# Kernel tuning notes

Measured on AMD Instinct MI355X. Metric: run time of the kernel, lower is better.

The kernel has to match this reference:

```python
import jax, jax.numpy as jnp
import numpy as np

# ---- Mamba2 / model hyperparameters (from init_kwargs + mamba_ssm defaults) ----
D_MODEL = 64
D_STATE = 64
D_CONV = 4
EXPAND = 2
HEADDIM = 64                      # mamba_ssm Mamba2 default
D_INNER = EXPAND * D_MODEL        # 128
NHEADS = D_INNER // HEADDIM       # 2
CONV_DIM = D_INNER + 2 * D_STATE  # 256 (ngroups=1)
D_IN_PROJ = 2 * D_INNER + 2 * D_STATE + NHEADS  # 386
B, T, F_ = 4, 128, 128
EPS = 1e-5


def silu(x):
    return x * jax.nn.sigmoid(x)


def depthwise_causal_conv(x, w, b):
    # x: [N, L, C], w: [C, K], b: [C]  (causal depthwise conv, as in Mamba2)
    xt = x.transpose(0, 2, 1)           # [N, C, L]
    kernel = w[:, None, :]              # [C, 1, K]
    y = jax.lax.conv_general_dilated(
        xt, kernel, window_strides=(1,), padding=[(D_CONV - 1, 0)],
        feature_group_count=CONV_DIM)
    return y.transpose(0, 2, 1) + b     # [N, L, C]


def mamba2(u, Wp, cw, cb, dtb, Al, Dp, nw, Wo):
    # u: [N, L, D_MODEL]
    Nb, L, _ = u.shape
    zxbcdt = u @ Wp.T                                   # [N, L, D_IN_PROJ]
    z = zxbcdt[..., :D_INNER]
    xBC = zxbcdt[..., D_INNER:D_INNER + CONV_DIM]
    dt = jax.nn.softplus(zxbcdt[..., -NHEADS:] + dtb)   # [N, L, H]
    xBC = silu(depthwise_causal_conv(xBC, cw, cb))
    x = xBC[..., :D_INNER].reshape(Nb, L, NHEADS, HEADDIM)
    Bm = xBC[..., D_INNER:D_INNER + D_STATE]            # [N, L, Nst]
    Cm = xBC[..., D_INNER + D_STATE:]                   # [N, L, Nst]
    dA = jnp.exp(dt * (-jnp.exp(Al)))                   # [N, L, H]

    def step(h, inp):
        # h: [N, H, P, Nst]
        dA_t, dt_t, x_t, B_t, C_t = inp
        h = h * dA_t[:, :, None, None] + (dt_t[:, :, None] * x_t)[..., None] * B_t[:, None, None, :]
        y = jnp.einsum('bhpn,bn->bhp', h, C_t)
        return h, y

    h0 = jnp.zeros((Nb, NHEADS, HEADDIM, D_STATE), u.dtype)
    xs = (dA.transpose(1, 0, 2), dt.transpose(1, 0, 2),
          x.transpose(1, 0, 2, 3), Bm.transpose(1, 0, 2), Cm.transpose(1, 0, 2))
    _, ys = jax.lax.scan(step, h0, xs)                  # ys: [L, N, H, P]
    y = ys.transpose(1, 0, 2, 3) + Dp[None, None, :, None] * x
    y = y.reshape(Nb, L, D_INNER)
    # RMSNormGated (norm_before_gate=False): gate then rms-normalize
    g = y * silu(z)
    g = g * jax.lax.rsqrt(jnp.mean(g * g, axis=-1, keepdims=True) + EPS) * nw
    return g @ Wo.T                                     # [N, L, D_MODEL]


def bimamba(u, p_fwd, p_bwd, fW, fb):
    out_f = mamba2(u, *p_fwd)
    out_b = mamba2(u[:, ::-1], *p_bwd)[:, ::-1]
    return jnp.concatenate([out_f, out_b], axis=-1) @ fW.T + fb


def layernorm(x, w, b):
    m = jnp.mean(x, axis=-1, keepdims=True)
    v = jnp.mean((x - m) ** 2, axis=-1, keepdims=True)
    return (x - m) * jax.lax.rsqrt(v + EPS) * w + b


def setup_inputs() -> dict:
    key = jax.random.key(0)
    ks = jax.random.split(key, 12)
    inp = {
        'x': jax.random.normal(ks[0], (B, D_MODEL, T, F_), jnp.float32),
        # 4 Mamba2 instances stacked: [freq_fwd, freq_bwd, time_fwd, time_bwd]
        'in_proj_W': 0.02 * jax.random.normal(ks[1], (4, D_IN_PROJ, D_MODEL), jnp.float32),
        'conv_W': 0.1 * jax.random.normal(ks[2], (4, CONV_DIM, D_CONV), jnp.float32),
        'conv_b': jnp.zeros((4, CONV_DIM), jnp.float32),
        'dt_bias': 0.1 * jax.random.normal(ks[3], (4, NHEADS), jnp.float32),
        'A_log': jnp.log(jax.random.uniform(ks[4], (4, NHEADS), jnp.float32, 1.0, 16.0)),
        'D_param': 0.1 * jax.random.normal(ks[5], (4, NHEADS), jnp.float32),
        'norm_w': jnp.ones((4, D_INNER), jnp.float32),
        'out_W': 0.02 * jax.random.normal(ks[6], (4, D_MODEL, D_INNER), jnp.float32),
        # 2 BiMamba fusion linears: [freq, time]
        'fusion_W': 0.02 * jax.random.normal(ks[7], (2, D_MODEL, 2 * D_MODEL), jnp.float32),
        'fusion_b': jnp.zeros((2, D_MODEL), jnp.float32),
        # 2 LayerNorms: [freq, time]
        'ln_w': jnp.ones((2, D_MODEL), jnp.float32),
        'ln_b': jnp.zeros((2, D_MODEL), jnp.float32),
    }
    return inp


def reference(x, in_proj_W, conv_W, conv_b, dt_bias, A_log, D_param, norm_w, out_W,
              fusion_W, fusion_b, ln_w, ln_b):
    Bb, Cc, Tt, Ff = x.shape

    def mp(i):
        return (in_proj_W[i], conv_W[i], conv_b[i], dt_bias[i], A_log[i],
                D_param[i], norm_w[i], out_W[i])

    # ---- frequency axis scan (dilation == 1) ----
    x_freq = x.transpose(0, 2, 3, 1).reshape(Bb * Tt, Ff, Cc)
    xf_out = bimamba(layernorm(x_freq, ln_w[0], ln_b[0]), mp(0), mp(1), fusion_W[0], fusion_b[0])
    x = x + xf_out.reshape(Bb, Tt, Ff, Cc).transpose(0, 3, 1, 2)

    # ---- time axis scan ----
    x_time = x.transpose(0, 3, 2, 1).reshape(Bb * Ff, Tt, Cc)
    xt_out = bimamba(layernorm(x_time, ln_w[1], ln_b[1]), mp(2), mp(3), fusion_W[1], fusion_b[1])
    x = x + xt_out.reshape(Bb, Ff, Tt, Cc).transpose(0, 3, 2, 1)
    return x
```

## Files before the change

kernel.cpp:

```cpp
#include <hip/hip_runtime.h>

#define EPSV 1e-5f

typedef short bf16x8 __attribute__((ext_vector_type(8)));
typedef float f32x4 __attribute__((ext_vector_type(4)));

__device__ __forceinline__ float sigmoidf_(float x) {
  return 1.f / (1.f + __expf(-x));
}
__device__ __forceinline__ unsigned short f2bf(float f) {
  unsigned int u = __float_as_uint(f);
  u += 0x7fffu + ((u >> 16) & 1u);
  return (unsigned short)(u >> 16);
}
__device__ __forceinline__ float bfu(unsigned short h) {
  union { unsigned int u; float f; } t; t.u = ((unsigned int)h) << 16; return t.f;
}
__device__ __forceinline__ float bflo(unsigned int u) {
  union { unsigned int x; float f; } t; t.x = u << 16; return t.f;
}
__device__ __forceinline__ float bfhi(unsigned int u) {
  union { unsigned int x; float f; } t; t.x = u & 0xffff0000u; return t.f;
}

__global__ __launch_bounds__(256) void precomp_wc(
    const float* __restrict__ fW,
    const float* __restrict__ oW,
    float* __restrict__ Wc)
{
  const int bi = blockIdx.x;
  const int i = bi >> 3, mg = bi & 7;
  const int m = (mg << 3) + (threadIdx.x >> 5);
  const int k0 = (threadIdx.x & 31) << 2;
  const int p = i >> 1, d = i & 1;
  const float* fr = fW + p * 8192 + m * 128 + d * 64;
  const float* orow = oW + i * 8192 + k0;
  float a0 = 0.f, a1 = 0.f, a2 = 0.f, a3 = 0.f;
  for (int j = 0; j < 64; ++j) {
    const float f = fr[j];
    const float4 o4 = *(const float4*)(orow + j * 128);
    a0 += f * o4.x; a1 += f * o4.y; a2 += f * o4.z; a3 += f * o4.w;
  }
  float* out = Wc + i * 8192 + m * 128 + k0;
  out[0] = a0; out[1] = a1; out[2] = a2; out[3] = a3;
}

__global__ __launch_bounds__(256) void precomp_wcf(
    const float* __restrict__ Wc, unsigned short* __restrict__ WcF)
{
  const int ip = blockIdx.x;
  const float* src = Wc + (size_t)ip * 8192;
  unsigned short* dst = WcF + (size_t)ip * 8192;
  for (int idx = threadIdx.x; idx < 8192; idx += 256) {
    const int tile = idx >> 11;
    const int h = (idx >> 9) & 3;
    const int lane = (idx >> 3) & 63;
    const int j = idx & 7;
    const int col = lane & 15, quad = lane >> 4;
    dst[idx] = f2bf(src[(tile * 16 + col) * 128 + h * 32 + quad * 8 + j]);
  }
}

__global__ __launch_bounds__(256) void precomp_wpf(
    const float* __restrict__ Wp, unsigned short* __restrict__ WpF)
{
  const int ip = blockIdx.x;
  const float* src = Wp + (size_t)ip * 24704;
  unsigned short* dst = WpF + (size_t)ip * 25600;
  for (int idx = threadIdx.x; idx < 25600; idx += 256) {
    const int tile = idx >> 10;
    const int rem = idx & 1023;
    const int h = rem >> 9;
    const int lane = (rem >> 3) & 63;
    const int j = idx & 7;
    const int col = lane & 15, quad = lane >> 4;
    const int o = tile * 16 + col;
    const int k = h * 32 + quad * 8 + j;
    dst[idx] = (o < 386) ? f2bf(src[o * 64 + k]) : (unsigned short)0;
  }
}

__global__ __launch_bounds__(256) void transp0(
    const float* __restrict__ x, float* __restrict__ x0)
{
  __shared__ float T[64 * 132];
  const int tid = threadIdx.x, blk = blockIdx.x;
  const int b = blk >> 7, t = blk & 127;
  {
    const int c = tid >> 2, f0 = (tid & 3) << 5;
    const float* xp = x + (((size_t)(b * 64 + c) * 128 + t) << 7) + f0;
    float* tp = &T[c * 132 + f0];
    #pragma unroll
    for (int j = 0; j < 8; ++j)
      *(float4*)(tp + (j << 2)) = *(const float4*)(xp + (j << 2));
  }
  __syncthreads();
  {
    const int f = tid >> 1, cb = (tid & 1) << 5;
    float* op = x0 + (((size_t)(b * 128 + t) * 128 + f) << 6) + cb;
    #pragma unroll
    for (int j = 0; j < 32; j += 4) {
      float4 v;
      v.x = T[(cb + j + 0) * 132 + f];
      v.y = T[(cb + j + 1) * 132 + f];
      v.z = T[(cb + j + 2) * 132 + f];
      v.w = T[(cb + j + 3) * 132 + f];
      *(float4*)(op + j) = v;
    }
  }
}

__global__ __launch_bounds__(512, 4) void mamba_dir(
    const float* __restrict__ src,
    unsigned short* __restrict__ ybuf,
    const unsigned short* __restrict__ WpF,
    const unsigned short* __restrict__ WcF,
    const float* __restrict__ cwA, const float* __restrict__ cbA,
    const float* __restrict__ dtbA, const float* __restrict__ AlA,
    const float* __restrict__ DpA, const float* __restrict__ nwA,
    const float* __restrict__ lnwA, const float* __restrict__ lnbA,
    int phase)
{
  __shared__ __align__(16) unsigned short sU[16 * 72];
  __shared__ __align__(16) unsigned short sZb[16 * 136];
  __shared__ __align__(16) float sZx[16 * 260];
  __shared__ __align__(16) unsigned short sBC16[16 * 136];
  __shared__ __align__(16) unsigned short sXdT[128 * 40];
  __shared__ __align__(16) unsigned short sXwT[128 * 40];
  __shared__ __align__(16) unsigned short sBT[64 * 40];
  __shared__ __align__(16) unsigned short sSm[2 * 16 * 40];
  __shared__ __align__(16) unsigned short sH[2 * 64 * 72];
  __shared__ float sMeta[16][2][4];
  __shared__ float sDtRaw[16][2];

  const int tid = threadIdx.x;
  const int blk = blockIdx.x;
  const int seq = blk >> 1, dir = blk & 1;
  const int ip = (phase << 1) + dir;
  const float dtb0 = dtbA[ip * 2], dtb1 = dtbA[ip * 2 + 1];
  const float nA0 = -__expf(AlA[ip * 2]), nA1 = -__expf(AlA[ip * 2 + 1]);
  const float Dp0 = DpA[ip * 2], Dp1 = DpA[ip * 2 + 1];
  const int c256 = tid & 255;
  const int lh = tid >> 8;
  float ch0 = 0.f, ch1 = 0.f, ch2 = 0.f;

  const int wv = tid >> 6, lane = tid & 63;
  const int col = lane & 15, quad = lane >> 4;

  f32x4 hacc[8];
  #pragma unroll
  for (int i = 0; i < 8; ++i) hacc[i] = (f32x4){0.f, 0.f, 0.f, 0.f};

  {
    unsigned int* z;
    z = (unsigned int*)sXdT; for (int i = tid; i < 2560; i += 512) z[i] = 0u;
    z = (unsigned int*)sXwT; for (int i = tid; i < 2560; i += 512) z[i] = 0u;
    z = (unsigned int*)sBT;  for (int i = tid; i < 1280; i += 512) z[i] = 0u;
    z = (unsigned int*)sSm;  for (int i = tid; i < 640;  i += 512) z[i] = 0u;
    z = (unsigned int*)sH;   for (int i = tid; i < 4608; i += 512) z[i] = 0u;
  }

  const unsigned short* wf = WpF + (size_t)ip * 25600;
  const unsigned short* wcf = WcF + (size_t)ip * 8192;
  const size_t sb = (size_t)seq << 13;
  const int pos = tid >> 6, lc = tid & 63;

  float vc0, vc1;
  {
    const int p0 = dir ? (127 - pos) : pos;
    const int p1 = dir ? (127 - (pos + 8)) : (pos + 8);
    vc0 = src[sb + (size_t)p0 * 64 + lc];
    vc1 = src[sb + (size_t)p1 * 64 + lc];
  }

  for (int ck = 0; ck < 8; ++ck) {
    float vn0 = 0.f, vn1 = 0.f;
    if (ck < 7) {
      const int st0 = ((ck + 1) << 4) + pos;
      const int p0 = dir ? (127 - st0) : st0;
      const int p1 = dir ? (127 - (st0 + 8)) : (st0 + 8);
      vn0 = src[sb + (size_t)p0 * 64 + lc];
      vn1 = src[sb + (size_t)p1 * 64 + lc];
    }
    {
      const int lnb_i = (phase << 6) + lc;
      const float lnw_v = lnwA[lnb_i], lnb_v = lnbA[lnb_i];
      #pragma unroll
      for (int half = 0; half < 2; ++half) {
        const float v = half ? vc1 : vc0;
        float sm = v, s2 = v * v;
        sm += __shfl_xor(sm, 1);  s2 += __shfl_xor(s2, 1);
        sm += __shfl_xor(sm, 2);  s2 += __shfl_xor(s2, 2);
        sm += __shfl_xor(sm, 4);  s2 += __shfl_xor(s2, 4);
        sm += __shfl_xor(sm, 8);  s2 += __shfl_xor(s2, 8);
        sm += __shfl_xor(sm, 16); s2 += __shfl_xor(s2, 16);
        sm += __shfl_xor(sm, 32); s2 += __shfl_xor(s2, 32);
        const float mean = sm * (1.f / 64.f);
        const float inv = rsqrtf(s2 * (1.f / 64.f) - mean * mean + EPSV);
        sU[(pos + half * 8) * 72 + lc] = f2bf((v - mean) * inv * lnw_v + lnb_v);
      }
    }
    __syncthreads();
    {
      const int wave = tid >> 6;
      const bf16x8 a0 = *(const bf16x8*)(&sU[col * 72 + quad * 8]);
      const bf16x8 a1 = *(const bf16x8*)(&sU[col * 72 + quad * 8 + 32]);
      for (int tile = wave; tile < 25; tile += 8) {
        const unsigned short* wt = wf + (tile << 10) + (lane << 3);
        const bf16x8 b0 = *(const bf16x8*)(wt);
        const bf16x8 b1 = *(const bf16x8*)(wt + 512);
        f32x4 d = {0.f, 0.f, 0.f, 0.f};
        d = __builtin_amdgcn_mfma_f32_16x16x32_bf16(a0, b0, d, 0, 0, 0);
        d = __builtin_amdgcn_mfma_f32_16x16x32_bf16(a1, b1, d, 0, 0, 0);
        const int o = (tile << 4) + col;
        if (tile < 8) {
          #pragma unroll
          for (int r = 0; r < 4; ++r)
            sZb[(quad * 4 + r) * 136 + o] = f2bf(d[r]);
        } else if (tile < 24) {
          #pragma unroll
          for (int r = 0; r < 4; ++r)
            sZx[(quad * 4 + r) * 260 + (o - 128)] = d[r];
        } else if (col < 2) {
          #pragma unroll
          for (int r = 0; r < 4; ++r)
            sDtRaw[quad * 4 + r][col] = d[r];
        }
      }
    }
    __syncthreads();
    {
      const int c = c256;
      const float4 cw4 = *(const float4*)(cwA + ip * 1024 + (c << 2));
      const float cbias = cbA[ip * 256 + c];
      float a0c, a1c, a2c;
      if (lh == 0) { a0c = ch0; a1c = ch1; a2c = ch2; }
      else {
        a0c = sZx[5 * 260 + c];
        a1c = sZx[6 * 260 + c];
        a2c = sZx[7 * 260 + c];
      }
      const int lt0 = lh << 3;
      unsigned int pkv[4];
      #pragma unroll
      for (int l = 0; l < 8; ++l) {
        const int lt = lt0 + l;
        const float a3 = sZx[lt * 260 + c];
        const float acc = cbias + a0c * cw4.x + a1c * cw4.y + a2c * cw4.z + a3 * cw4.w;
        const float sv = acc * sigmoidf_(acc);
        const unsigned int hv = (unsigned int)f2bf(sv);
        if (c >= 192)      sBC16[lt * 136 + 64 + (c - 192)] = (unsigned short)hv;
        else if (c >= 128) sBC16[lt * 136 + (c - 128)] = (unsigned short)hv;
        if (l & 1) pkv[l >> 1] |= hv << 16; else pkv[l >> 1] = hv;
        a0c = a1c; a1c = a2c; a2c = a3;
      }
      if (c < 128)
        *(uint4*)(&sXdT[c * 40 + lt0]) = make_uint4(pkv[0], pkv[1], pkv[2], pkv[3]);
      else if (c < 192)
        *(uint4*)(&sBT[(c - 128) * 40 + lt0]) = make_uint4(pkv[0], pkv[1], pkv[2], pkv[3]);
      if (lh == 0) {
        ch0 = sZx[13 * 260 + c];
        ch1 = sZx[14 * 260 + c];
        ch2 = sZx[15 * 260 + c];
      }
      if (tid < 32) {
        const int lt = tid >> 1, hh = tid & 1;
        const float rawv = sDtRaw[lt][hh] + (hh ? dtb1 : dtb0);
        const float dtv = (rawv > 20.f) ? rawv : log1pf(__expf(rawv));
        float Lx = dtv * (hh ? nA1 : nA0);
        #pragma unroll
        for (int d = 2; d < 32; d <<= 1) {
          const float tpv = __shfl_up(Lx, d);
          Lx += (tid >= d) ? tpv : 0.f;
        }
        const float Ltot = __shfl(Lx, 30 + hh);
        *(float4*)(&sMeta[lt][hh][0]) =
            make_float4(Lx, dtv, __expf(Ltot - Lx) * dtv, __expf(Lx));
      }
    }
    __syncthreads();
    f32x4 yD0, yD1;
    if (wv == 0) {
      const bf16x8 ca0 = *(const bf16x8*)(&sBC16[col * 136 + 64 + quad * 8]);
      const bf16x8 ca1 = *(const bf16x8*)(&sBC16[col * 136 + 96 + quad * 8]);
      const bf16x8 bb0 = *(const bf16x8*)(&sBC16[col * 136 + quad * 8]);
      const bf16x8 bb1 = *(const bf16x8*)(&sBC16[col * 136 + 32 + quad * 8]);
      f32x4 g = {0.f, 0.f, 0.f, 0.f};
      g = __builtin_amdgcn_mfma_f32_16x16x32_bf16(ca0, bb0, g, 0, 0, 0);
      g = __builtin_amdgcn_mfma_f32_16x16x32_bf16(ca1, bb1, g, 0, 0, 0);
      #pragma unroll
      for (int h = 0; h < 2; ++h) {
        const float Ls = sMeta[col][h][0];
        const float dts = sMeta[col][h][1];
        #pragma unroll
        for (int r = 0; r < 4; ++r) {
          const int t = quad * 4 + r;
          const float m = (col <= t) ? __expf(sMeta[t][h][0] - Ls) * dts : 0.f;
          sSm[(h * 16 + t) * 40 + col] = f2bf(g[r] * m);
        }
      }
    } else if (wv <= 2) {
      if (ck < 7) {
        const int p = ((wv - 1) << 6) + lane;
        const int hh = p >> 6;
        #pragma unroll
        for (int tp = 0; tp < 8; ++tp) {
          const unsigned int xr = *(const unsigned int*)(&sXdT[p * 40 + tp * 2]);
          const unsigned int lo = (unsigned int)f2bf(bflo(xr) * sMeta[tp * 2][hh][2]);
          const unsigned int hi = (unsigned int)f2bf(bfhi(xr) * sMeta[tp * 2 + 1][hh][2]);
          *(unsigned int*)(&sXwT[p * 40 + tp * 2]) = lo | (hi << 16);
        }
      }
    } else if (wv >= 4) {
      const int h = (wv - 4) >> 1, pt2 = (wv - 4) & 1;
      const bf16x8 ca0 = *(const bf16x8*)(&sBC16[col * 136 + 64 + quad * 8]);
      const bf16x8 ca1 = *(const bf16x8*)(&sBC16[col * 136 + 96 + quad * 8]);
      const unsigned short* hp0 = &sH[(h * 64 + pt2 * 32 + col) * 72];
      const unsigned short* hp1 = hp0 + 16 * 72;
      const bf16x8 h00 = *(const bf16x8*)(hp0 + quad * 8);
      const bf16x8 h01 = *(const bf16x8*)(hp0 + 32 + quad * 8);
      const bf16x8 h10 = *(const bf16x8*)(hp1 + quad * 8);
      const bf16x8 h11 = *(const bf16x8*)(hp1 + 32 + quad * 8);
      yD0 = (f32x4){0.f, 0.f, 0.f, 0.f};
      yD1 = (f32x4){0.f, 0.f, 0.f, 0.f};
      yD0 = __builtin_amdgcn_mfma_f32_16x16x32_bf16(ca0, h00, yD0, 0, 0, 0);
      yD0 = __builtin_amdgcn_mfma_f32_16x16x32_bf16(ca1, h01, yD0, 0, 0, 0);
      yD1 = __builtin_amdgcn_mfma_f32_16x16x32_bf16(ca0, h10, yD1, 0, 0, 0);
      yD1 = __builtin_amdgcn_mfma_f32_16x16x32_bf16(ca1, h11, yD1, 0, 0, 0);
      #pragma unroll
      for (int r = 0; r < 4; ++r) {
        const float Pv = sMeta[quad * 4 + r][h][3];
        yD0[r] *= Pv; yD1[r] *= Pv;
      }
    }
    __syncthreads();
    if (wv < 4) {
      if (ck < 7) {
        const int h = wv >> 1, ph = wv & 1;
        const int pb = h * 64 + ph * 32;
        const float At = sMeta[15][h][3];
        const bf16x8 xa0 = *(const bf16x8*)(&sXwT[(pb + col) * 40 + quad * 8]);
        const bf16x8 xa1 = *(const bf16x8*)(&sXwT[(pb + 16 + col) * 40 + quad * 8]);
        #pragma unroll
        for (int nt = 0; nt < 4; ++nt) {
          const bf16x8 bbt = *(const bf16x8*)(&sBT[(nt * 16 + col) * 40 + quad * 8]);
          #pragma unroll
          for (int r = 0; r < 4; ++r) { hacc[nt][r] *= At; hacc[nt + 4][r] *= At; }
          hacc[nt]     = __builtin_amdgcn_mfma_f32_16x16x32_bf16(xa0, bbt, hacc[nt], 0, 0, 0);
          hacc[nt + 4] = __builtin_amdgcn_mfma_f32_16x16x32_bf16(xa1, bbt, hacc[nt + 4], 0, 0, 0);
        }
        #pragma unroll
        for (int nt = 0; nt < 4; ++nt) {
          #pragma unroll
          for (int r = 0; r < 4; ++r) {
            sH[(pb + quad * 4 + r) * 72 + nt * 16 + col] = f2bf(hacc[nt][r]);
            sH[(pb + 16 + quad * 4 + r) * 72 + nt * 16 + col] = f2bf(hacc[nt + 4][r]);
          }
        }
      }
    } else {
      const int h = (wv - 4) >> 1, pt2 = (wv - 4) & 1;
      const int cb0 = h * 64 + pt2 * 32;
      const float dp = h ? Dp1 : Dp0;
      const bf16x8 sa = *(const bf16x8*)(&sSm[(h * 16 + col) * 40 + quad * 8]);
      const bf16x8 xb0 = *(const bf16x8*)(&sXdT[(cb0 + col) * 40 + quad * 8]);
      const bf16x8 xb1 = *(const bf16x8*)(&sXdT[(cb0 + 16 + col) * 40 + quad * 8]);
      yD0 = __builtin_amdgcn_mfma_f32_16x16x32_bf16(sa, xb0, yD0, 0, 0, 0);
      yD1 = __builtin_amdgcn_mfma_f32_16x16x32_bf16(sa, xb1, yD1, 0, 0, 0);
      const uint2 xw0 = *(const uint2*)(&sXdT[(cb0 + col) * 40 + quad * 4]);
      const uint2 xw1 = *(const uint2*)(&sXdT[(cb0 + 16 + col) * 40 + quad * 4]);
      yD0[0] += dp * bflo(xw0.x); yD0[1] += dp * bfhi(xw0.x);
      yD0[2] += dp * bflo(xw0.y); yD0[3] += dp * bfhi(xw0.y);
      yD1[0] += dp * bflo(xw1.x); yD1[1] += dp * bfhi(xw1.x);
      yD1[2] += dp * bflo(xw1.y); yD1[3] += dp * bfhi(xw1.y);
      #pragma unroll
      for (int r = 0; r < 4; ++r) {
        sZx[(quad * 4 + r) * 260 + cb0 + col] = yD0[r];
        sZx[(quad * 4 + r) * 260 + cb0 + 16 + col] = yD1[r];
      }
    }
    __syncthreads();
    {
      const int w = tid >> 6, kk = tid & 63, k0 = kk << 1;
      const float2 nw2 = *(const float2*)(nwA + ip * 128 + k0);
      #pragma unroll
      for (int sub = 0; sub < 2; ++sub) {
        const int lt = w + (sub << 3);
        const float2 yv = *(const float2*)(&sZx[lt * 260 + k0]);
        const unsigned int zp = *(const unsigned int*)(&sZb[lt * 136 + k0]);
        const float z0 = bflo(zp), z1 = bfhi(zp);
        const float g0 = yv.x * (z0 * sigmoidf_(z0));
        const float g1 = yv.y * (z1 * sigmoidf_(z1));
        float ssq = g0 * g0 + g1 * g1;
        ssq += __shfl_xor(ssq, 1);
        ssq += __shfl_xor(ssq, 2);
        ssq += __shfl_xor(ssq, 4);
        ssq += __shfl_xor(ssq, 8);
        ssq += __shfl_xor(ssq, 16);
        ssq += __shfl_xor(ssq, 32);
        const float sc = rsqrtf(ssq * (1.f / 128.f) + EPSV);
        const unsigned int lo = f2bf(g0 * sc * nw2.x);
        const unsigned int hi = f2bf(g1 * sc * nw2.y);
        *(unsigned int*)(&sZb[lt * 136 + k0]) = lo | (hi << 16);
      }
    }
    __syncthreads();
    {
      const int wave = tid >> 6;
      if (wave < 4) {
        const unsigned short* wt = wcf + (wave << 11);
        f32x4 d = {0.f, 0.f, 0.f, 0.f};
        #pragma unroll
        for (int h = 0; h < 4; ++h) {
          const bf16x8 a = *(const bf16x8*)(&sZb[col * 136 + (h << 5) + (quad << 3)]);
          const bf16x8 bb = *(const bf16x8*)(wt + (h << 9) + (lane << 3));
          d = __builtin_amdgcn_mfma_f32_16x16x32_bf16(a, bb, d, 0, 0, 0);
        }
        const size_t yb = ((size_t)(dir * 512 + seq) * 128) << 6;
        #pragma unroll
        for (int r = 0; r < 4; ++r) {
          const int pp = (quad << 2) + r;
          const int st = (ck << 4) + pp, rp = dir ? (127 - st) : st;
          ybuf[yb + ((size_t)rp << 6) + (wave << 4) + col] = f2bf(d[r]);
        }
      }
    }
    vc0 = vn0; vc1 = vn1;
  }
}

__global__ __launch_bounds__(256) void combine0(
    const float* __restrict__ x, const unsigned short* __restrict__ ybuf,
    const float* __restrict__ fb, float* __restrict__ x1)
{
  __shared__ float T[64 * 132];
  const int tid = threadIdx.x, blk = blockIdx.x;
  const int b = blk >> 7, t = blk & 127;
  {
    const int c = tid >> 2, f0 = (tid & 3) << 5;
    const float* xp = x + (((size_t)(b * 64 + c) * 128 + t) << 7) + f0;
    float* tp = &T[c * 132 + f0];
    #pragma unroll
    for (int j = 0; j < 8; ++j)
      *(float4*)(tp + (j << 2)) = *(const float4*)(xp + (j << 2));
  }
  __syncthreads();
  {
    const int f = tid >> 1, cb = (tid & 1) << 5;
    const size_t s0 = (size_t)b * 128 + t;
    const unsigned short* yf = ybuf + ((s0 * 128 + f) << 6) + cb;
    const unsigned short* yb = ybuf + (((s0 + 512) * 128 + f) << 6) + cb;
    float* op = x1 + (((size_t)(b * 128 + f) * 128 + t) << 6) + cb;
    #pragma unroll
    for (int j = 0; j < 32; j += 4) {
      float4 v;
      v.x = T[(cb + j + 0) * 132 + f] + bfu(yf[j + 0]) + bfu(yb[j + 0]) + fb[cb + j + 0];
      v.y = T[(cb + j + 1) * 132 + f] + bfu(yf[j + 1]) + bfu(yb[j + 1]) + fb[cb + j + 1];
      v.z = T[(cb + j + 2) * 132 + f] + bfu(yf[j + 2]) + bfu(yb[j + 2]) + fb[cb + j + 2];
      v.w = T[(cb + j + 3) * 132 + f] + bfu(yf[j + 3]) + bfu(yb[j + 3]) + fb[cb + j + 3];
      *(float4*)(op + j) = v;
    }
  }
}

__global__ __launch_bounds__(256) void combine1(
    const float* __restrict__ x1, const unsigned short* __restrict__ ybuf,
    const float* __restrict__ fb, float* __restrict__ out)
{
  __shared__ float T[128 * 68];
  const int tid = threadIdx.x, blk = blockIdx.x;
  const int b = blk >> 7, t = blk & 127;
  {
    const int f = tid >> 1, cb = (tid & 1) << 5;
    const size_t s1 = (size_t)b * 128 + f;
    const float* xp = x1 + ((s1 * 128 + t) << 6) + cb;
    const unsigned short* yf = ybuf + ((s1 * 128 + t) << 6) + cb;
    const unsigned short* yb = ybuf + (((s1 + 512) * 128 + t) << 6) + cb;
    float* tp = &T[f * 68 + cb];
    #pragma unroll
    for (int j = 0; j < 32; j += 4) {
      const float4 xv = *(const float4*)(xp + j);
      const uint2 yfv = *(const uint2*)(yf + j);
      const uint2 ybv = *(const uint2*)(yb + j);
      const float4 fv = *(const float4*)(fb + cb + j);
      tp[j + 0] = xv.x + bflo(yfv.x) + bflo(ybv.x) + fv.x;
      tp[j + 1] = xv.y + bfhi(yfv.x) + bfhi(ybv.x) + fv.y;
      tp[j + 2] = xv.z + bflo(yfv.y) + bflo(ybv.y) + fv.z;
      tp[j + 3] = xv.w + bfhi(yfv.y) + bfhi(ybv.y) + fv.w;
    }
  }
  __syncthreads();
  {
    const int c = tid >> 2, f0 = (tid & 3) << 5;
    float* op = out + (((size_t)(b * 64 + c) * 128 + t) << 7) + f0;
    #pragma unroll
    for (int j = 0; j < 32; j += 4) {
      float4 v;
      v.x = T[(f0 + j + 0) * 68 + c];
      v.y = T[(f0 + j + 1) * 68 + c];
      v.z = T[(f0 + j + 2) * 68 + c];
      v.w = T[(f0 + j + 3) * 68 + c];
      *(float4*)(op + j) = v;
    }
  }
}

extern "C" void kernel_launch(void* const* d_in, const int* in_sizes, int n_in,
                              void* d_out, int out_size, void* d_ws, size_t ws_size,
                              hipStream_t stream) {
  const float* x   = (const float*)d_in[0];
  const float* Wp  = (const float*)d_in[1];
  const float* cw  = (const float*)d_in[2];
  const float* cb  = (const float*)d_in[3];
  const float* dtb = (const float*)d_in[4];
  const float* Al  = (const float*)d_in[5];
  const float* Dp  = (const float*)d_in[6];
  const float* nw  = (const float*)d_in[7];
  const float* oW  = (const float*)d_in[8];
  const float* fW  = (const float*)d_in[9];
  const float* fb  = (const float*)d_in[10];
  const float* lnw = (const float*)d_in[11];
  const float* lnb = (const float*)d_in[12];

  float* ws = (float*)d_ws;
  float* Wc = ws;
  unsigned short* WpF = (unsigned short*)(ws + 32768);
  unsigned short* WcF = (unsigned short*)(ws + 32768 + 51200);
  float* xbuf = ws + 32768 + 51200 + 16384;
  unsigned short* y = (unsigned short*)(xbuf + 4194304);

  precomp_wc<<<32, 256, 0, stream>>>(fW, oW, Wc);
  precomp_wcf<<<4, 256, 0, stream>>>(Wc, WcF);
  precomp_wpf<<<4, 256, 0, stream>>>(Wp, WpF);
  transp0<<<512, 256, 0, stream>>>(x, xbuf);
  mamba_dir<<<1024, 512, 0, stream>>>(xbuf, y, WpF, WcF, cw, cb, dtb, Al, Dp,
                                      nw, lnw, lnb, 0);
  combine0<<<512, 256, 0, stream>>>(x, y, fb, xbuf);
  mamba_dir<<<1024, 512, 0, stream>>>(xbuf, y, WpF, WcF, cw, cb, dtb, Al, Dp,
                                      nw, lnw, lnb, 1);
  combine1<<<512, 256, 0, stream>>>(xbuf, y, fb + 64, (float*)d_out);
}
```

Baseline: 400.1 us.

## Spread chunked SSM state update across all eight waves

Measured after the change: 382.2 us. -4.5%, faster.

```diff
diff --git a/kernel.cpp b/kernel.cpp
--- a/kernel.cpp
+++ b/kernel.cpp
@@ -147,9 +147,9 @@
   const int wv = tid >> 6, lane = tid & 63;
   const int col = lane & 15, quad = lane >> 4;
 
-  f32x4 hacc[8];
+  f32x4 hacc[4];
   #pragma unroll
-  for (int i = 0; i < 8; ++i) hacc[i] = (f32x4){0.f, 0.f, 0.f, 0.f};
+  for (int i = 0; i < 4; ++i) hacc[i] = (f32x4){0.f, 0.f, 0.f, 0.f};
 
   {
     unsigned int* z;
@@ -202,10 +202,9 @@
     }
     __syncthreads();
     {
-      const int wave = tid >> 6;
       const bf16x8 a0 = *(const bf16x8*)(&sU[col * 72 + quad * 8]);
       const bf16x8 a1 = *(const bf16x8*)(&sU[col * 72 + quad * 8 + 32]);
-      for (int tile = wave; tile < 25; tile += 8) {
+      for (int tile = wv; tile < 25; tile += 8) {
         const unsigned short* wt = wf + (tile << 10) + (lane << 3);
         const bf16x8 b0 = *(const bf16x8*)(wt);
         const bf16x8 b1 = *(const bf16x8*)(wt + 512);
@@ -279,7 +278,6 @@
       }
     }
     __syncthreads();
-    f32x4 yD0, yD1;
     if (wv == 0) {
       const bf16x8 ca0 = *(const bf16x8*)(&sBC16[col * 136 + 64 + quad * 8]);
       const bf16x8 ca1 = *(const bf16x8*)(&sBC16[col * 136 + 96 + quad * 8]);
@@ -313,79 +311,76 @@
       }
     } else if (wv >= 4) {
       const int h = (wv - 4) >> 1, pt2 = (wv - 4) & 1;
-      const bf16x8 ca0 = *(const bf16x8*)(&sBC16[col * 136 + 64 + quad * 8]);
-      const bf16x8 ca1 = *(const bf16x8*)(&sBC16[col * 136 + 96 + quad * 8]);
-      const unsigned short* hp0 = &sH[(h * 64 + pt2 * 32 + col) * 72];
-      const unsigned short* hp1 = hp0 + 16 * 72;
-      const bf16x8 h00 = *(const bf16x8*)(hp0 + quad * 8);
-      const bf16x8 h01 = *(const bf16x8*)(hp0 + 32 + quad * 8);
-      const bf16x8 h10 = *(const bf16x8*)(hp1 + quad * 8);
-      const bf16x8 h11 = *(const bf16x8*)(hp1 + 32 + quad * 8);
-      yD0 = (f32x4){0.f, 0.f, 0.f, 0.f};
-      yD1 = (f32x4){0.f, 0.f, 0.f, 0.f};
-      yD0 = __builtin_amdgcn_mfma_f32_16x16x32_bf16(ca0, h00, yD0, 0, 0, 0);
-      yD0 = __builtin_amdgcn_mfma_f32_16x16x32_bf16(ca1, h01, yD0, 0, 0, 0);
-      yD1 = __builtin_amdgcn_mfma_f32_16x16x32_bf16(ca0, h10, yD1, 0, 0, 0);
-      yD1 = __builtin_amdgcn_mfma_f32_16x16x32_bf16(ca1, h11, yD1, 0, 0, 0);
-      #pragma unroll
-      for (int r = 0; r < 4; ++r) {
-        const float Pv = sMeta[quad * 4 + r][h][3];
-        yD0[r] *= Pv; yD1[r] *= Pv;
-      }
-    }
-    __syncthreads();
-    if (wv < 4) {
-      if (ck < 7) {
-        const int h = wv >> 1, ph = wv & 1;
-        const int pb = h * 64 + ph * 32;
-        const float At = sMeta[15][h][3];
-        const bf16x8 xa0 = *(const bf16x8*)(&sXwT[(pb + col) * 40 + quad * 8]);
-        const bf16x8 xa1 = *(const bf16x8*)(&sXwT[(pb + 16 + col) * 40 + quad * 8]);
-        #pragma unroll
-        for (int nt = 0; nt < 4; ++nt) {
-          const bf16x8 bbt = *(const bf16x8*)(&sBT[(nt * 16 + col) * 40 + quad * 8]);
+      const int cb0 = h * 64 + pt2 * 32;
+      if (ck) {
+        const bf16x8 ca0 = *(const bf16x8*)(&sBC16[col * 136 + 64 + quad * 8]);
+        const bf16x8 ca1 = *(const bf16x8*)(&sBC16[col * 136 + 96 + quad * 8]);
+        #pragma unroll
+        for (int half = 0; half < 2; ++half) {
+          const unsigned short* hp = &sH[(cb0 + half * 16 + col) * 72];
+          const bf16x8 h0 = *(const bf16x8*)(hp + quad * 8);
+          const bf16x8 h1 = *(const bf16x8*)(hp + 32 + quad * 8);
+          f32x4 d = {0.f, 0.f, 0.f, 0.f};
+          d = __builtin_amdgcn_mfma_f32_16x16x32_bf16(ca0, h0, d, 0, 0, 0);
+          d = __builtin_amdgcn_mfma_f32_16x16x32_bf16(ca1, h1, d, 0, 0, 0);
           #pragma unroll
-          for (int r = 0; r < 4; ++r) { hacc[nt][r] *= At; hacc[nt + 4][r] *= At; }
-          hacc[nt]     = __builtin_amdgcn_mfma_f32_16x16x32_bf16(xa0, bbt, hacc[nt], 0, 0, 0);
-          hacc[nt + 4] = __builtin_amdgcn_mfma_f32_16x16x32_bf16(xa1, bbt, hacc[nt + 4], 0, 0, 0);
-        }
-        #pragma unroll
-        for (int nt = 0; nt < 4; ++nt) {
-          #pragma unroll
-          for (int r = 0; r < 4; ++r) {
-            sH[(pb + quad * 4 + r) * 72 + nt * 16 + col] = f2bf(hacc[nt][r]);
-            sH[(pb + 16 + quad * 4 + r) * 72 + nt * 16 + col] = f2bf(hacc[nt + 4][r]);
-          }
-        }
-      }
-    } else {
-      const int h = (wv - 4) >> 1, pt2 = (wv - 4) & 1;
-      const int cb0 = h * 64 + pt2 * 32;
+          for (int r = 0; r < 4; ++r)
+            sZx[(quad * 4 + r) * 260 + cb0 + half * 16 + col] =
+                d[r] * sMeta[quad * 4 + r][h][3];
+        }
+      } else {
+        #pragma unroll
+        for (int r = 0; r < 4; ++r) {
+          sZx[(quad * 4 + r) * 260 + cb0 + col] = 0.f;
+          sZx[(quad * 4 + r) * 260 + cb0 + 16 + col] = 0.f;
+        }
+      }
+    }
+    __syncthreads();
+    if (ck < 7) {
+      const int h = wv >> 2;
+      const int pb = wv << 4;
+      const float At = sMeta[15][h][3];
+      const bf16x8 xa = *(const bf16x8*)(&sXwT[(pb + col) * 40 + quad * 8]);
+      #pragma unroll
+      for (int nt = 0; nt < 4; ++nt) {
+        const bf16x8 bbt = *(const bf16x8*)(&sBT[(nt * 16 + col) * 40 + quad * 8]);
+        #pragma unroll
+        for (int r = 0; r < 4; ++r) hacc[nt][r] *= At;
+        hacc[nt] = __builtin_amdgcn_mfma_f32_16x16x32_bf16(xa, bbt, hacc[nt], 0, 0, 0);
+      }
+      #pragma unroll
+      for (int nt = 0; nt < 4; ++nt) {
+        #pragma unroll
+        for (int r = 0; r < 4; ++r)
+          sH[(pb + quad * 4 + r) * 72 + nt * 16 + col] = f2bf(hacc[nt][r]);
+      }
+    }
+    __syncthreads();
+    {
+      const int h = wv >> 2;
+      const int c = (wv << 4) + col;
       const float dp = h ? Dp1 : Dp0;
       const bf16x8 sa = *(const bf16x8*)(&sSm[(h * 16 + col) * 40 + quad * 8]);
-      const bf16x8 xb0 = *(const bf16x8*)(&sXdT[(cb0 + col) * 40 + quad * 8]);
-      const bf16x8 xb1 = *(const bf16x8*)(&sXdT[(cb0 + 16 + col) * 40 + quad * 8]);
-      yD0 = __builtin_amdgcn_mfma_f32_16x16x32_bf16(sa, xb0, yD0, 0, 0, 0);
-      yD1 = __builtin_amdgcn_mfma_f32_16x16x32_bf16(sa, xb1, yD1, 0, 0, 0);
-      const uint2 xw0 = *(const uint2*)(&sXdT[(cb0 + col) * 40 + quad * 4]);
-      const uint2 xw1 = *(const uint2*)(&sXdT[(cb0 + 16 + col) * 40 + quad * 4]);
-      yD0[0] += dp * bflo(xw0.x); yD0[1] += dp * bfhi(xw0.x);
-      yD0[2] += dp * bflo(xw0.y); yD0[3] += dp * bfhi(xw0.y);
-      yD1[0] += dp * bflo(xw1.x); yD1[1] += dp * bfhi(xw1.x);
-      yD1[2] += dp * bflo(xw1.y); yD1[3] += dp * bfhi(xw1.y);
-      #pragma unroll
-      for (int r = 0; r < 4; ++r) {
-        sZx[(quad * 4 + r) * 260 + cb0 + col] = yD0[r];
-        sZx[(quad * 4 + r) * 260 + cb0 + 16 + col] = yD1[r];
-      }
+      const bf16x8 xb = *(const bf16x8*)(&sXdT[c * 40 + quad * 8]);
+      f32x4 cin;
+      #pragma unroll
+      for (int r = 0; r < 4; ++r) cin[r] = sZx[(quad * 4 + r) * 260 + c];
+      f32x4 yD = __builtin_amdgcn_mfma_f32_16x16x32_bf16(sa, xb, cin, 0, 0, 0);
+      const uint2 xw = *(const uint2*)(&sXdT[c * 40 + quad * 4]);
+      yD[0] += dp * bflo(xw.x); yD[1] += dp * bfhi(xw.x);
+      yD[2] += dp * bflo(xw.y); yD[3] += dp * bfhi(xw.y);
+      #pragma unroll
+      for (int r = 0; r < 4; ++r)
+        sZx[(quad * 4 + r) * 260 + c] = yD[r];
     }
     __syncthreads();
     {
-      const int w = tid >> 6, kk = tid & 63, k0 = kk << 1;
+      const int k0 = lc << 1;
       const float2 nw2 = *(const float2*)(nwA + ip * 128 + k0);
       #pragma unroll
       for (int sub = 0; sub < 2; ++sub) {
-        const int lt = w + (sub << 3);
+        const int lt = wv + (sub << 3);
         const float2 yv = *(const float2*)(&sZx[lt * 260 + k0]);
         const unsigned int zp = *(const unsigned int*)(&sZb[lt * 136 + k0]);
         const float z0 = bflo(zp), z1 = bfhi(zp);
@@ -406,9 +401,8 @@
     }
     __syncthreads();
     {
-      const int wave = tid >> 6;
-      if (wave < 4) {
-        const unsigned short* wt = wcf + (wave << 11);
+      if (wv < 4) {
+        const unsigned short* wt = wcf + (wv << 11);
         f32x4 d = {0.f, 0.f, 0.f, 0.f};
         #pragma unroll
         for (int h = 0; h < 4; ++h) {
@@ -421,7 +415,7 @@
         for (int r = 0; r < 4; ++r) {
           const int pp = (quad << 2) + r;
           const int st = (ck << 4) + pp, rp = dir ? (127 - st) : st;
-          ybuf[yb + ((size_t)rp << 6) + (wave << 4) + col] = f2bf(d[r]);
+          ybuf[yb + ((size_t)rp << 6) + (wv << 4) + col] = f2bf(d[r]);
         }
       }
     }
```
